# Kernel optimization log

Measured on AMD Instinct MI355X. Metric: run time of the kernel, lower is better.

Reference implementation:

```python
import jax, jax.numpy as jnp
import numpy as np

K = 20          # n_knn
BN_EPS = 1e-5   # torch BatchNorm2d default eps


def knn_idx(x, k):
    # x: (B, C, N). pairwise[b,i,j] = -||x_i||^2 + 2 x_i.x_j - ||x_j||^2 (neg sq dist)
    xx = jnp.sum(x * x, axis=1)                      # (B, N)
    inner = jnp.einsum('bci,bcj->bij', x, x)          # (B, N, N)
    pd = 2.0 * inner - xx[:, :, None] - xx[:, None, :]
    return jax.lax.top_k(pd, k)[1]                    # (B, N, k) nearest (incl. self)


def setup_inputs() -> dict:
    key = jax.random.key(0)
    k1, k2, k3, k4 = jax.random.split(key, 4)
    B, C, N, O = 8, 64, 2048, 128
    x = jax.random.normal(k1, (B, C, N), dtype=jnp.float32)
    W = jax.random.normal(k2, (O, 2 * C), dtype=jnp.float32) * 0.05  # conv1x1 weight, no bias
    gamma = 1.0 + 0.1 * jax.random.normal(k3, (O,), dtype=jnp.float32)
    beta = 0.1 * jax.random.normal(k4, (O,), dtype=jnp.float32)
    return {'x': x, 'W': W, 'gamma': gamma, 'beta': beta}


def reference(x, W, gamma, beta):
    # x: (B, C, N)
    idx = knn_idx(x, K)                               # (B, N, K) int32
    xt = jnp.swapaxes(x, 1, 2)                        # (B, N, C)
    nbr = jax.vmap(lambda xb, ib: xb[ib])(xt, idx)    # (B, N, K, C) gathered neighbors
    center = xt[:, :, None, :]                        # (B, N, 1, C)
    feat = jnp.concatenate(
        [nbr - center, jnp.broadcast_to(center, nbr.shape)], axis=-1
    )                                                 # (B, N, K, 2C)
    # 1x1 conv == per-edge GEMM
    h = jnp.einsum('bnkc,oc->bnko', feat, W)          # (B, N, K, O)
    # BatchNorm2d (training mode): batch stats over (B, N, K) per channel, biased var
    mean = jnp.mean(h, axis=(0, 1, 2))
    var = jnp.var(h, axis=(0, 1, 2))
    h = (h - mean) * jax.lax.rsqrt(var + BN_EPS) * gamma + beta
    h = jax.nn.gelu(h, approximate=False)             # torch nn.GELU exact erf form
    out = jnp.max(h, axis=2)                          # max over k neighbors -> (B, N, O)
    return jnp.swapaxes(out, 1, 2)                    # (B, O, N) matches torch layout
```

## Files before the change

### kernel.cpp

```cpp
#include <hip/hip_runtime.h>
#include <math.h>

#define BB 8
#define CC 64
#define NN 2048
#define KK 20
#define OO 128
#define CANDT 28
#define NPART 512
#define NPARTB 1024
#define M_TOT 327680.0f

typedef __attribute__((ext_vector_type(8))) __bf16 bf8v;
typedef __attribute__((ext_vector_type(16))) float f32x16;

__global__ __launch_bounds__(256, 4) void k_pqprep(const float* __restrict__ x,
                                                   const float* __restrict__ W,
                                                   float* __restrict__ P,
                                                   float* __restrict__ Q,
                                                   ushort* __restrict__ xT,
                                                   float* __restrict__ xTf,
                                                   double* __restrict__ xx,
                                                   float* __restrict__ xxf) {
  __shared__ float xs[32][68];
  __shared__ float Wl[OO][68];
  __shared__ float tile[32][OO + 1];
  const int t = threadIdx.x;
  const int jj = t & 31, og = t >> 5;
  const int pt0 = blockIdx.x * 32;
  const int b = pt0 >> 11;
  const int n0 = pt0 & (NN - 1);

#pragma unroll
  for (int r = 0; r < 2; ++r) {
    int seg = t + r * 256;
    int c = seg >> 3, n4 = (seg & 7) * 4;
    float4 v = *(const float4*)(x + ((size_t)(b * CC + c) << 11) + n0 + n4);
    xs[n4 + 0][c] = v.x; xs[n4 + 1][c] = v.y;
    xs[n4 + 2][c] = v.z; xs[n4 + 3][c] = v.w;
  }
#pragma unroll
  for (int r = 0; r < 8; ++r) {
    int seg = t + r * 256;
    int o = seg >> 4, c4 = (seg & 15) * 4;
    *(float4*)(&Wl[o][c4]) = *(const float4*)(W + (size_t)o * (2 * CC) + c4);
  }
  __syncthreads();

  float xcol[CC];
#pragma unroll
  for (int c = 0; c < CC; c += 4) {
    float4 v = *(const float4*)(&xs[jj][c]);
    xcol[c] = v.x; xcol[c + 1] = v.y; xcol[c + 2] = v.z; xcol[c + 3] = v.w;
  }

  if (t < 32) {
    int i = pt0 + t;
    ushort* rowp = xT + (size_t)i * CC;
    float* rowf = xTf + (size_t)i * CC;
    double s = 0.0;
#pragma unroll
    for (int c8 = 0; c8 < 8; ++c8) {
      unsigned tmp[8];
      float f[8];
#pragma unroll
      for (int e = 0; e < 8; ++e) {
        float v = xs[t][c8 * 8 + e];
// ... 96 lines not shown
    pk.w = tmp[6] | (tmp[7] << 16);
    *(uint4*)(rowp + c8 * 8) = pk;
    *(float4*)(rowf + c8 * 8)     = make_float4(f[0], f[1], f[2], f[3]);
    *(float4*)(rowf + c8 * 8 + 4) = make_float4(f[4], f[5], f[6], f[7]);
  }
  xx[i] = s;
  xxf[i] = (float)s;
}

__global__ __launch_bounds__(256) void k_pq(const float* __restrict__ x,
                                            const float* __restrict__ W,
                                            float* __restrict__ P,
                                            float* __restrict__ Q) {
  __shared__ float tile[64][OO + 1];
  const int t = threadIdx.x;
  const int jj = t & 63, og = t >> 6;
  const int pt0 = blockIdx.x * 64;
  const int b = pt0 >> 11;
  const int jn = (pt0 & (NN - 1)) + jj;

  float xcol[CC];
#pragma unroll
  for (int c = 0; c < CC; ++c) xcol[c] = x[((size_t)(b * CC + c) << 11) + jn];

  for (int oo = 0; oo < 32; ++oo) {
    int o = og * 32 + oo;
    const float* wr = W + (size_t)o * (2 * CC);
    float sp = 0.f;
#pragma unroll
    for (int c = 0; c < CC; ++c) sp = fmaf(wr[c], xcol[c], sp);
    tile[jj][o] = sp;
  }
  __syncthreads();
  for (int it = 0; it < 32; ++it) {
    int r = it * 2 + (t >> 7);
    P[((size_t)(pt0 + r)) * OO + (t & 127)] = tile[r][t & 127];
  }
  __syncthreads();
  for (int oo = 0; oo < 32; ++oo) {
    int o = og * 32 + oo;
    const float* wr = W + (size_t)o * (2 * CC);
    float sq = 0.f;
#pragma unroll
    for (int c = 0; c < CC; ++c) sq = fmaf(wr[CC + c] - wr[c], xcol[c], sq);
    tile[jj][o] = sq;
  }
  __syncthreads();
  for (int it = 0; it < 32; ++it) {
    int r = it * 2 + (t >> 7);
    Q[((size_t)(pt0 + r)) * OO + (t & 127)] = tile[r][t & 127];
  }
}

__global__ __launch_bounds__(1024, 4) void k_knn(
    const ushort* __restrict__ xT, const float* __restrict__ xxf,
    const float* __restrict__ xTf, const double* __restrict__ xx,
    int* __restrict__ idx, const float* __restrict__ P,
    const float* __restrict__ Q, float* __restrict__ partial,
    float* __restrict__ vmaxA, float* __restrict__ vminA) {
  extern __shared__ char smem[];
  ushort (*Sb)[NN] = (ushort(*)[NN])smem;
  int* Cj = (int*)(smem + 32 * NN * 2);
  double* Sd = (double*)(smem + 32 * NN * 2 + 4096);
  float* redF = (float*)Sd;
  int (*sIdxL)[KK] = (int(*)[KK])(smem + 32 * NN * 2 + 4096 + 8192);
  const int t = threadIdx.x;
  const int w = t >> 6, lane = t & 63;
  const int bidswz = ((blockIdx.x & 7) << 6) + (blockIdx.x >> 3);
  const int b = bidswz >> 6;
  const int i0 = (bidswz & 63) << 5;
  const int lr = lane & 31, lh = lane >> 5;
  const ushort* xTb = xT + (((size_t)b) << 11) * CC;

  f32x16 acc[4];
#pragma unroll
  for (int tt = 0; tt < 4; ++tt)
#pragma unroll
    for (int q = 0; q < 16; ++q) acc[tt][q] = 0.f;

  const ushort* Ap = xTb + (size_t)(i0 + lr) * CC + lh * 8;
  bf8v a0 = *(const bf8v*)(Ap);
  bf8v a1 = *(const bf8v*)(Ap + 16);
  bf8v a2 = *(const bf8v*)(Ap + 32);
  bf8v a3 = *(const bf8v*)(Ap + 48);
  const int j0w = w << 7;
#pragma unroll
  for (int tt = 0; tt < 4; ++tt) {
    const ushort* Bp = xTb + (size_t)(j0w + tt * 32 + lr) * CC + lh * 8;
    bf8v b0 = *(const bf8v*)(Bp);
    bf8v b1 = *(const bf8v*)(Bp + 16);
    bf8v b2 = *(const bf8v*)(Bp + 32);
    bf8v b3 = *(const bf8v*)(Bp + 48);
    acc[tt] = __builtin_amdgcn_mfma_f32_32x32x16_bf16(a0, b0, acc[tt], 0, 0, 0);
    acc[tt] = __builtin_amdgcn_mfma_f32_32x32x16_bf16(a1, b1, acc[tt], 0, 0, 0);
    acc[tt] = __builtin_amdgcn_mfma_f32_32x32x16_bf16(a2, b2, acc[tt], 0, 0, 0);
    acc[tt] = __builtin_amdgcn_mfma_f32_32x32x16_bf16(a3, b3, acc[tt], 0, 0, 0);
  }

  const float* xxfb = xxf + (b << 11);
#pragma unroll
  for (int tt = 0; tt < 4; ++tt) {
    int j = j0w + tt * 32 + lr;
    float xv = xxfb[j];
#pragma unroll
    for (int q = 0; q < 16; ++q) {
      int rr = (q & 3) + 8 * (q >> 2) + 4 * lh;
      float sv = fmaf(2.f, acc[tt][q], -xv);
      unsigned u = __float_as_uint(sv);
      u ^= (0x80000000u | (unsigned)((int)u >> 31));
      Sb[rr][j] = (ushort)(u >> 16);
    }
  }
  __syncthreads();

  const float* xTfb = xTf + (((size_t)b) << 11) * CC;
  const double* xxb = xx + (b << 11);
#pragma unroll 1
  for (int rw = 0; rw < 2; ++rw) {
    const int rr = w + 16 * rw;
    const int irow = i0 + rr;
    uint4 kq[4];
    unsigned t0 = 0, t1 = 0, t2 = 0, t3 = 0;
#pragma unroll
    for (int g = 0; g < 4; ++g) {
      uint4 raw = *(const uint4*)(&Sb[rr][lane * 8 + g * 512]);
      kq[g] = raw;
      const unsigned wds[4] = {raw.x, raw.y, raw.z, raw.w};
#pragma unroll
      for (int e = 0; e < 4; ++e) {
        unsigned k0 = wds[e] & 0xffffu, k1 = wds[e] >> 16;
        unsigned mx, mn;
        mx = k0 > t0 ? k0 : t0; mn = k0 > t0 ? t0 : k0; t0 = mx;
        mx = mn > t1 ? mn : t1; mn = mn > t1 ? t1 : mn; t1 = mx;
        mx = mn > t2 ? mn : t2; mn = mn > t2 ? t2 : mn; t2 = mx;
        t3 = mn > t3 ? mn : t3;
        mx = k1 > t0 ? k1 : t0; mn = k1 > t0 ? t0 : k1; t0 = mx;
        mx = mn > t1 ? mn : t1; mn = mn > t1 ? t1 : mn; t1 = mx;
        mx = mn > t2 ? mn : t2; mn = mn > t2 ? t2 : mn; t2 = mx;
        t3 = mn > t3 ? mn : t3;
      }
    }
    unsigned tau = 0;
    for (int bit = 15; bit >= 0; --bit) {
      unsigned cnd = tau | (1u << bit);
      int tot = __popcll(__ballot(t0 >= cnd)) + __popcll(__ballot(t1 >= cnd)) +
                __popcll(__ballot(t2 >= cnd)) + __popcll(__ballot(t3 >= cnd));
      if (tot >= CANDT) tau = cnd;
    }
    unsigned mask = 0;
#pragma unroll
    for (int g = 0; g < 4; ++g) {
      const unsigned wds[4] = {kq[g].x, kq[g].y, kq[g].z, kq[g].w};
#pragma unroll
      for (int e = 0; e < 4; ++e) {
        mask |= ((wds[e] & 0xffffu) >= tau ? 1u : 0u) << (g * 8 + e * 2);
        mask |= ((wds[e] >> 16) >= tau ? 1u : 0u) << (g * 8 + e * 2 + 1);
      }
    }
    int myc = __popc(mask);
    int pre = myc;
#pragma unroll
    for (int off = 1; off < 64; off <<= 1) {
      int o = __shfl_up(pre, off, 64);
      pre += (lane >= off) ? o : 0;
    }
    int tot = __shfl(pre, 63, 64);
    if (tot > 64) {
      tau = 0;
      for (int bit = 15; bit >= 0; --bit) {
        unsigned cnd = tau | (1u << bit);
        int cc = 0;
#pragma unroll
        for (int g = 0; g < 4; ++g) {
          const unsigned wds[4] = {kq[g].x, kq[g].y, kq[g].z, kq[g].w};
#pragma unroll
          for (int e = 0; e < 4; ++e) {
            cc += ((wds[e] & 0xffffu) >= cnd) ? 1 : 0;
            cc += ((wds[e] >> 16) >= cnd) ? 1 : 0;
          }
        }
#pragma unroll
        for (int off = 1; off < 64; off <<= 1) cc += __shfl_xor(cc, off, 64);
        if (cc >= CANDT) tau = cnd;
      }
      mask = 0;
#pragma unroll
      for (int g = 0; g < 4; ++g) {
        const unsigned wds[4] = {kq[g].x, kq[g].y, kq[g].z, kq[g].w};
#pragma unroll
        for (int e = 0; e < 4; ++e) {
          mask |= ((wds[e] & 0xffffu) >= tau ? 1u : 0u) << (g * 8 + e * 2);
          mask |= ((wds[e] >> 16) >= tau ? 1u : 0u) << (g * 8 + e * 2 + 1);
        }
      }
      myc = __popc(mask);
      pre = myc;
#pragma unroll
      for (int off = 1; off < 64; off <<= 1) {
        int o = __shfl_up(pre, off, 64);
        pre += (lane >= off) ? o : 0;
      }
      tot = __shfl(pre, 63, 64);
    }
    {
      int slot = pre - myc;
      unsigned m2 = mask;
      while (m2) {
        int bp = __builtin_ctz(m2); m2 &= m2 - 1;
        if (slot < 64) Cj[w * 64 + slot] = lane * 8 + ((bp >> 3) << 9) + (bp & 7);
        ++slot;
      }
    }
    int cnt = tot > 64 ? 64 : tot;
    int j = Cj[w * 64 + (lane < cnt ? lane : 0)];
    const float* xi = xTfb + (size_t)irow * CC;
    const float* xj = xTfb + (size_t)j * CC;
    double d0 = 0, d1 = 0, d2 = 0, d3 = 0;
#pragma unroll
    for (int c = 0; c < CC; c += 4) {
      float4 fi = *(const float4*)(xi + c);
      float4 fj = *(const float4*)(xj + c);
      d0 = fma((double)fi.x, (double)fj.x, d0);
      d1 = fma((double)fi.y, (double)fj.y, d1);
      d2 = fma((double)fi.z, (double)fj.z, d2);
      d3 = fma((double)fi.w, (double)fj.w, d3);
    }
    double sc = 2.0 * ((d0 + d1) + (d2 + d3)) - xxb[j];
    Sd[w * 64 + lane] = sc;
    int rank = 0;
#pragma unroll 4
    for (int mm = 0; mm < cnt; ++mm) {
      double sm = Sd[w * 64 + mm];
      int jm = Cj[w * 64 + mm];
      rank += (sm > sc || (sm == sc && jm < j)) ? 1 : 0;
    }
    if (lane < cnt && rank < KK) {
      idx[(size_t)((b << 11) + irow) * KK + rank] = j;
      sIdxL[rr][rank] = j;
    }
  }

  if (P != nullptr) {
    __syncthreads();
    const int grp = t >> 7;
    const int o = t & 127;
    float s = 0.f, s2 = 0.f;
#pragma unroll
    for (int pp = 0; pp < 4; ++pp) {
      const int pl = grp * 4 + pp;
      const int pt = (b << 11) + i0 + pl;
      float qv = Q[(size_t)pt * OO + o];
      float vmax = -3.0e38f, vmin = 3.0e38f;
#pragma unroll
      for (int k = 0; k < KK; ++k) {
        float v = P[((size_t)((b << 11) + sIdxL[pl][k])) * OO + o] + qv;
        s += v;
        s2 = fmaf(v, v, s2);
        vmax = fmaxf(vmax, v);
        vmin = fminf(vmin, v);
      }
      vmaxA[(size_t)pt * OO + o] = vmax;
      vminA[(size_t)pt * OO + o] = vmin;
    }
    redF[grp * 128 + o] = s;
    redF[1024 + grp * 128 + o] = s2;
    __syncthreads();
    if (t < 128) {
      float as = 0.f, as2 = 0.f;
#pragma unroll
      for (int g = 0; g < 8; ++g) {
        as  += redF[g * 128 + t];
        as2 += redF[1024 + g * 128 + t];
      }
      partial[(size_t)bidswz * 128 + t]               = as;
      partial[(size_t)NPART * 128 + (size_t)bidswz * 128 + t] = as2;
    }
  }
}

__global__ __launch_bounds__(256) void k_stats(const float* __restrict__ P,
                                               const float* __restrict__ Q,
                                               const int* __restrict__ idx,
                                               float* __restrict__ partial) {
  __shared__ int sIdx[16 * KK];
  __shared__ float red[512];
  const int t = threadIdx.x;
  const int o = t & 127, half = t >> 7;
  const int bid = (blockIdx.x & 7) * 128 + (blockIdx.x >> 3);
  const int pt0 = bid * 16;
  const int b = pt0 >> 11;
  if (t < 160)
    *(int2*)(sIdx + t * 2) = *(const int2*)(idx + (size_t)pt0 * KK + t * 2);
  __syncthreads();

  float s = 0.f, s2 = 0.f;
  for (int it = 0; it < 8; ++it) {
    int pl = it * 2 + half;
    int pt = pt0 + pl;
    float qv = Q[(size_t)pt * OO + o];
    const int* ip = sIdx + pl * KK;
#pragma unroll
    for (int k = 0; k < KK; ++k) {
// ... 53 lines not shown
  const float scale = ss[o], shift = ss[128 + o];
  const int pt0 = bid * 32;
  const int b = pt0 >> 11;
  const float inv_sqrt2 = 0.70710678118654752f;
  for (int it = 0; it < 16; ++it) {
    int pl = it * 2 + half;
    int pt = pt0 + pl;
    float vmax, vmin;
    if (use_minmax) {
      vmax = vmaxA[(size_t)pt * OO + o];
      vmin = vminA[(size_t)pt * OO + o];
    } else {
      float qv = Q[(size_t)pt * OO + o];
      const int* ip = idx + (size_t)pt * KK;
      vmax = -3.0e38f; vmin = 3.0e38f;
#pragma unroll
      for (int k = 0; k < KK; ++k) {
        float v = P[((size_t)((b << 11) + ip[k])) * OO + o] + qv;
        vmax = fmaxf(vmax, v);
        vmin = fminf(vmin, v);
      }
    }
    float ymax, ymin;
    if (scale >= 0.f) { ymax = fmaf(vmax, scale, shift); ymin = fmaf(vmin, scale, shift); }
    else              { ymax = fmaf(vmin, scale, shift); ymin = fmaf(vmax, scale, shift); }
    float g;
    if (ymax > 0.f) {
      g = 0.5f * ymax * (1.0f + erff(ymax * inv_sqrt2));
    } else {
      float g1 = 0.5f * ymax * (1.0f + erff(ymax * inv_sqrt2));
      float g2 = 0.5f * ymin * (1.0f + erff(ymin * inv_sqrt2));
      g = fmaxf(g1, g2);
    }
    tile[pl][o] = g;
  }
  __syncthreads();
  const int n0 = pt0 & (NN - 1);
  for (int rep = 0; rep < 16; ++rep) {
    int oo = rep * 8 + (t >> 5);
    int nn = t & 31;
    out[((size_t)(b * OO + oo) << 11) + n0 + nn] = tile[nn][oo];
  }
}

extern "C" void kernel_launch(void* const* d_in, const int* in_sizes, int n_in,
                              void* d_out, int out_size, void* d_ws, size_t ws_size,
                              hipStream_t stream) {
  const float* x     = (const float*)d_in[0];
  const float* W     = (const float*)d_in[1];
  const float* gamma = (const float*)d_in[2];
  const float* beta  = (const float*)d_in[3];
  float* out = (float*)d_out;

  const int knn_lds = 32 * NN * 2 + 4096 + 8192 + 32 * KK * 4;
  hipFuncSetAttribute((const void*)k_knn,
                      hipFuncAttributeMaxDynamicSharedMemorySize, knn_lds);

  const size_t needA = 131072 + 65536 + 1310720 + (size_t)2 * NPARTB * 128 * 4 +
                       1024 + 4ull * 8388608;

  if (ws_size >= needA) {
    double* xx   = (double*)d_ws;
    float*  xxf  = (float*)(xx + BB * NN);
    int*    idxp = (int*)(xxf + BB * NN);
    float*  part = (float*)(idxp + (size_t)BB * NN * KK);
    float*  ss   = part + 2 * NPARTB * 128;
    float*  P    = ss + 256;
    float*  Q    = P + (size_t)BB * NN * OO;
    ushort* xT   = (ushort*)(Q + (size_t)BB * NN * OO);
    float*  xTf  = (float*)(xT + (size_t)BB * NN * CC);
    float*  vmax = xTf + (size_t)BB * NN * CC;
    float*  vmin = vmax + (size_t)BB * NN * OO;
    const size_t needSafe = (size_t)((char*)(vmin + (size_t)BB * NN * OO) - (char*)d_ws);
    if (ws_size >= needSafe) {
      hipLaunchKernelGGL(k_pqprep, dim3(BB * NN / 32), dim3(256), 0, stream,
                         x, W, P, Q, xT, xTf, xx, xxf);
      hipLaunchKernelGGL(k_knn, dim3(BB * NN / 32), dim3(1024), knn_lds, stream,
                         xT, xxf, xTf, xx, idxp, P, Q, part, vmax, vmin);
      hipLaunchKernelGGL(k_fin, dim3(128), dim3(256), 0, stream, part, gamma, beta, ss, NPART);
      hipLaunchKernelGGL(k_out, dim3(BB * NN / 32), dim3(256), 0, stream,
                         P, Q, idxp, ss, vmax, vmin, 1, out);
      return;
    }
    ushort* xTa  = (ushort*)(Q + (size_t)BB * NN * OO);
    float*  xTfa = (float*)(xTa + (size_t)BB * NN * CC);
    hipLaunchKernelGGL(k_pqprep, dim3(BB * NN / 32), dim3(256), 0, stream,
                       x, W, P, Q, xTa, xTfa, xx, xxf);
    hipLaunchKernelGGL(k_knn, dim3(BB * NN / 32), dim3(1024), knn_lds, stream,
                       xTa, xxf, xTfa, xx, idxp,
                       (const float*)nullptr, (const float*)nullptr,
                       (float*)nullptr, (float*)nullptr, (float*)nullptr);
    hipLaunchKernelGGL(k_stats, dim3(NPARTB), dim3(256), 0, stream,
                       P, Q, idxp, part);
    hipLaunchKernelGGL(k_fin, dim3(128), dim3(256), 0, stream, part, gamma, beta, ss, NPARTB);
    hipLaunchKernelGGL(k_out, dim3(BB * NN / 32), dim3(256), 0, stream,
                       P, Q, idxp, ss, (const float*)nullptr, (const float*)nullptr, 0, out);
  } else {
    double* xx   = (double*)d_ws;
    int*    idxp = (int*)(xx + BB * NN);
    float*  P    = (float*)(idxp + (size_t)BB * NN * KK);
    float*  Q    = P + (size_t)BB * NN * OO;
    float*  part = Q + (size_t)BB * NN * OO;
    float*  ss   = part + 2 * NPARTB * 128;
    ushort* xT   = (ushort*)P;
    float*  xTf  = P + (size_t)BB * NN * (CC / 2);
    float*  xxf  = Q;

    hipLaunchKernelGGL(k_prep, dim3(BB * NN / 256), dim3(256), 0, stream,
                       x, xT, xTf, xx, xxf);
    hipLaunchKernelGGL(k_knn, dim3(BB * NN / 32), dim3(1024), knn_lds, stream,
                       xT, xxf, xTf, xx, idxp,
                       (const float*)nullptr, (const float*)nullptr,
                       (float*)nullptr, (float*)nullptr, (float*)nullptr);
    hipLaunchKernelGGL(k_pq, dim3(BB * NN / 64), dim3(256), 0, stream, x, W, P, Q);
    hipLaunchKernelGGL(k_stats, dim3(NPARTB), dim3(256), 0, stream,
                       P, Q, idxp, part);
    hipLaunchKernelGGL(k_fin, dim3(128), dim3(256), 0, stream, part, gamma, beta, ss, NPARTB);
    hipLaunchKernelGGL(k_out, dim3(BB * NN / 32), dim3(256), 0, stream,
                       P, Q, idxp, ss, (const float*)nullptr, (const float*)nullptr, 0, out);
  }
}
```

Before: 115.6 us.

## Interleave two KNN rows per wave and split MFMA score tiles into halves

Each wave now processes its two query rows together, interleaving their top-4 filtering, radix threshold search, prefix sums, fp64 rescoring and rank computation to expose more instruction-level parallelism and hide LDS and global latency. The MFMA score computation is split into two halves of two accumulators each, lowering peak register pressure. Candidate and score buffers in LDS are doubled to hold per-row data, which raises LDS use and may lower occupancy. The interleaved code also raises register demand in the selection phase.

```diff
diff --git a/kernel.cpp b/kernel.cpp
--- a/kernel.cpp
+++ b/kernel.cpp
@@ -215,6 +215,45 @@
   }
 }
 
+__device__ __forceinline__ void exact_radix_q(const uint4* kq, int lane,
+                                              unsigned& tau, unsigned& mask,
+                                              int& myc, int& pre, int& tot) {
+  tau = 0;
+  for (int bit = 15; bit >= 0; --bit) {
+    unsigned cnd = tau | (1u << bit);
+    int cc = 0;
+#pragma unroll
+    for (int g = 0; g < 4; ++g) {
+      const unsigned wds[4] = {kq[g].x, kq[g].y, kq[g].z, kq[g].w};
+#pragma unroll
+      for (int e = 0; e < 4; ++e) {
+        cc += ((wds[e] & 0xffffu) >= cnd) ? 1 : 0;
+        cc += ((wds[e] >> 16) >= cnd) ? 1 : 0;
+      }
+    }
+#pragma unroll
+    for (int off = 1; off < 64; off <<= 1) cc += __shfl_xor(cc, off, 64);
+    if (cc >= CANDT) tau = cnd;
+  }
+  mask = 0;
+#pragma unroll
+  for (int g = 0; g < 4; ++g) {
+    const unsigned wds[4] = {kq[g].x, kq[g].y, kq[g].z, kq[g].w};
+#pragma unroll
+    for (int e = 0; e < 4; ++e) {
+      mask |= ((wds[e] & 0xffffu) >= tau ? 1u : 0u) << (g * 8 + e * 2);
+      mask |= ((wds[e] >> 16) >= tau ? 1u : 0u) << (g * 8 + e * 2 + 1);
+    }
+  }
+  myc = __popc(mask); pre = myc;
+#pragma unroll
+  for (int off = 1; off < 64; off <<= 1) {
+    int o = __shfl_up(pre, off, 64);
+    pre += (lane >= off) ? o : 0;
+  }
+  tot = __shfl(pre, 63, 64);
+}
+
 __global__ __launch_bounds__(1024, 4) void k_knn(
     const ushort* __restrict__ xT, const float* __restrict__ xxf,
     const float* __restrict__ xTf, const double* __restrict__ xx,
@@ -223,10 +262,10 @@
     float* __restrict__ vmaxA, float* __restrict__ vminA) {
   extern __shared__ char smem[];
   ushort (*Sb)[NN] = (ushort(*)[NN])smem;
-  int* Cj = (int*)(smem + 32 * NN * 2);
-  double* Sd = (double*)(smem + 32 * NN * 2 + 4096);
-  float* redF = (float*)Sd;
-  int (*sIdxL)[KK] = (int(*)[KK])(smem + 32 * NN * 2 + 4096 + 8192);
+  int (*CjS)[64] = (int(*)[64])(smem + 32 * NN * 2);
+  double (*SdS)[64] = (double(*)[64])(smem + 32 * NN * 2 + 8192);
+  float* redF = (float*)SdS;
+  int (*sIdxL)[KK] = (int(*)[KK])(smem + 32 * NN * 2 + 8192 + 16384);
   const int t = threadIdx.x;
   const int w = t >> 6, lane = t & 63;
   const int bidswz = ((blockIdx.x & 7) << 6) + (blockIdx.x >> 3);
@@ -234,12 +273,7 @@
   const int i0 = (bidswz & 63) << 5;
   const int lr = lane & 31, lh = lane >> 5;
   const ushort* xTb = xT + (((size_t)b) << 11) * CC;
-
-  f32x16 acc[4];
-#pragma unroll
-  for (int tt = 0; tt < 4; ++tt)
-#pragma unroll
-    for (int q = 0; q < 16; ++q) acc[tt][q] = 0.f;
+  const float* xxfb = xxf + (b << 11);
 
   const ushort* Ap = xTb + (size_t)(i0 + lr) * CC + lh * 8;
   bf8v a0 = *(const bf8v*)(Ap);
@@ -247,160 +281,183 @@
   bf8v a2 = *(const bf8v*)(Ap + 32);
   bf8v a3 = *(const bf8v*)(Ap + 48);
   const int j0w = w << 7;
-#pragma unroll
-  for (int tt = 0; tt < 4; ++tt) {
-    const ushort* Bp = xTb + (size_t)(j0w + tt * 32 + lr) * CC + lh * 8;
-    bf8v b0 = *(const bf8v*)(Bp);
-    bf8v b1 = *(const bf8v*)(Bp + 16);
-    bf8v b2 = *(const bf8v*)(Bp + 32);
-    bf8v b3 = *(const bf8v*)(Bp + 48);
-    acc[tt] = __builtin_amdgcn_mfma_f32_32x32x16_bf16(a0, b0, acc[tt], 0, 0, 0);
-    acc[tt] = __builtin_amdgcn_mfma_f32_32x32x16_bf16(a1, b1, acc[tt], 0, 0, 0);
-    acc[tt] = __builtin_amdgcn_mfma_f32_32x32x16_bf16(a2, b2, acc[tt], 0, 0, 0);
-    acc[tt] = __builtin_amdgcn_mfma_f32_32x32x16_bf16(a3, b3, acc[tt], 0, 0, 0);
-  }
-
-  const float* xxfb = xxf + (b << 11);
-#pragma unroll
-  for (int tt = 0; tt < 4; ++tt) {
-    int j = j0w + tt * 32 + lr;
-    float xv = xxfb[j];
-#pragma unroll
-    for (int q = 0; q < 16; ++q) {
-      int rr = (q & 3) + 8 * (q >> 2) + 4 * lh;
-      float sv = fmaf(2.f, acc[tt][q], -xv);
-      unsigned u = __float_as_uint(sv);
-      u ^= (0x80000000u | (unsigned)((int)u >> 31));
-      Sb[rr][j] = (ushort)(u >> 16);
+#pragma unroll 1
+  for (int h = 0; h < 2; ++h) {
+    f32x16 acc2[2];
+#pragma unroll
+    for (int u = 0; u < 2; ++u)
+#pragma unroll
+      for (int q = 0; q < 16; ++q) acc2[u][q] = 0.f;
+#pragma unroll
+    for (int u = 0; u < 2; ++u) {
+      const int tt = h * 2 + u;
+      const ushort* Bp = xTb + (size_t)(j0w + tt * 32 + lr) * CC + lh * 8;
+      bf8v b0 = *(const bf8v*)(Bp);
+      bf8v b1 = *(const bf8v*)(Bp + 16);
+      bf8v b2 = *(const bf8v*)(Bp + 32);
+      bf8v b3 = *(const bf8v*)(Bp + 48);
+      acc2[u] = __builtin_amdgcn_mfma_f32_32x32x16_bf16(a0, b0, acc2[u], 0, 0, 0);
+      acc2[u] = __builtin_amdgcn_mfma_f32_32x32x16_bf16(a1, b1, acc2[u], 0, 0, 0);
+      acc2[u] = __builtin_amdgcn_mfma_f32_32x32x16_bf16(a2, b2, acc2[u], 0, 0, 0);
+      acc2[u] = __builtin_amdgcn_mfma_f32_32x32x16_bf16(a3, b3, acc2[u], 0, 0, 0);
+    }
+#pragma unroll
+    for (int u = 0; u < 2; ++u) {
+      const int tt = h * 2 + u;
+      int j = j0w + tt * 32 + lr;
+      float xv = xxfb[j];
+#pragma unroll
+      for (int q = 0; q < 16; ++q) {
+        int rr = (q & 3) + 8 * (q >> 2) + 4 * lh;
+        float sv = fmaf(2.f, acc2[u][q], -xv);
+        unsigned uu = __float_as_uint(sv);
+        uu ^= (0x80000000u | (unsigned)((int)uu >> 31));
+        Sb[rr][j] = (ushort)(uu >> 16);
+      }
     }
   }
   __syncthreads();
 
   const float* xTfb = xTf + (((size_t)b) << 11) * CC;
   const double* xxb = xx + (b << 11);
-#pragma unroll 1
-  for (int rw = 0; rw < 2; ++rw) {
-    const int rr = w + 16 * rw;
-    const int irow = i0 + rr;
-    uint4 kq[4];
-    unsigned t0 = 0, t1 = 0, t2 = 0, t3 = 0;
-#pragma unroll
-    for (int g = 0; g < 4; ++g) {
-      uint4 raw = *(const uint4*)(&Sb[rr][lane * 8 + g * 512]);
-      kq[g] = raw;
-      const unsigned wds[4] = {raw.x, raw.y, raw.z, raw.w};
-#pragma unroll
-      for (int e = 0; e < 4; ++e) {
-        unsigned k0 = wds[e] & 0xffffu, k1 = wds[e] >> 16;
-        unsigned mx, mn;
-        mx = k0 > t0 ? k0 : t0; mn = k0 > t0 ? t0 : k0; t0 = mx;
-        mx = mn > t1 ? mn : t1; mn = mn > t1 ? t1 : mn; t1 = mx;
-        mx = mn > t2 ? mn : t2; mn = mn > t2 ? t2 : mn; t2 = mx;
-        t3 = mn > t3 ? mn : t3;
-        mx = k1 > t0 ? k1 : t0; mn = k1 > t0 ? t0 : k1; t0 = mx;
-        mx = mn > t1 ? mn : t1; mn = mn > t1 ? t1 : mn; t1 = mx;
-        mx = mn > t2 ? mn : t2; mn = mn > t2 ? t2 : mn; t2 = mx;
-        t3 = mn > t3 ? mn : t3;
-      }
-    }
-    unsigned tau = 0;
-    for (int bit = 15; bit >= 0; --bit) {
-      unsigned cnd = tau | (1u << bit);
-      int tot = __popcll(__ballot(t0 >= cnd)) + __popcll(__ballot(t1 >= cnd)) +
-                __popcll(__ballot(t2 >= cnd)) + __popcll(__ballot(t3 >= cnd));
-      if (tot >= CANDT) tau = cnd;
-    }
-    unsigned mask = 0;
-#pragma unroll
-    for (int g = 0; g < 4; ++g) {
-      const unsigned wds[4] = {kq[g].x, kq[g].y, kq[g].z, kq[g].w};
-#pragma unroll
-      for (int e = 0; e < 4; ++e) {
-        mask |= ((wds[e] & 0xffffu) >= tau ? 1u : 0u) << (g * 8 + e * 2);
-        mask |= ((wds[e] >> 16) >= tau ? 1u : 0u) << (g * 8 + e * 2 + 1);
-      }
-    }
-    int myc = __popc(mask);
-    int pre = myc;
-#pragma unroll
-    for (int off = 1; off < 64; off <<= 1) {
-      int o = __shfl_up(pre, off, 64);
-      pre += (lane >= off) ? o : 0;
-    }
-    int tot = __shfl(pre, 63, 64);
-    if (tot > 64) {
-      tau = 0;
-      for (int bit = 15; bit >= 0; --bit) {
-        unsigned cnd = tau | (1u << bit);
-        int cc = 0;
-#pragma unroll
-        for (int g = 0; g < 4; ++g) {
-          const unsigned wds[4] = {kq[g].x, kq[g].y, kq[g].z, kq[g].w};
-#pragma unroll
-          for (int e = 0; e < 4; ++e) {
-            cc += ((wds[e] & 0xffffu) >= cnd) ? 1 : 0;
-            cc += ((wds[e] >> 16) >= cnd) ? 1 : 0;
-          }
-        }
-#pragma unroll
-        for (int off = 1; off < 64; off <<= 1) cc += __shfl_xor(cc, off, 64);
-        if (cc >= CANDT) tau = cnd;
-      }
-      mask = 0;
-#pragma unroll
-      for (int g = 0; g < 4; ++g) {
-        const unsigned wds[4] = {kq[g].x, kq[g].y, kq[g].z, kq[g].w};
-#pragma unroll
-        for (int e = 0; e < 4; ++e) {
-          mask |= ((wds[e] & 0xffffu) >= tau ? 1u : 0u) << (g * 8 + e * 2);
-          mask |= ((wds[e] >> 16) >= tau ? 1u : 0u) << (g * 8 + e * 2 + 1);
-        }
-      }
-      myc = __popc(mask);
-      pre = myc;
-#pragma unroll
-      for (int off = 1; off < 64; off <<= 1) {
-        int o = __shfl_up(pre, off, 64);
-        pre += (lane >= off) ? o : 0;
-      }
-      tot = __shfl(pre, 63, 64);
-    }
-    {
-      int slot = pre - myc;
-      unsigned m2 = mask;
-      while (m2) {
-        int bp = __builtin_ctz(m2); m2 &= m2 - 1;
-        if (slot < 64) Cj[w * 64 + slot] = lane * 8 + ((bp >> 3) << 9) + (bp & 7);
-        ++slot;
-      }
-    }
-    int cnt = tot > 64 ? 64 : tot;
-    int j = Cj[w * 64 + (lane < cnt ? lane : 0)];
-    const float* xi = xTfb + (size_t)irow * CC;
-    const float* xj = xTfb + (size_t)j * CC;
-    double d0 = 0, d1 = 0, d2 = 0, d3 = 0;
-#pragma unroll
-    for (int c = 0; c < CC; c += 4) {
-      float4 fi = *(const float4*)(xi + c);
-      float4 fj = *(const float4*)(xj + c);
-      d0 = fma((double)fi.x, (double)fj.x, d0);
-      d1 = fma((double)fi.y, (double)fj.y, d1);
-      d2 = fma((double)fi.z, (double)fj.z, d2);
-      d3 = fma((double)fi.w, (double)fj.w, d3);
-    }
-    double sc = 2.0 * ((d0 + d1) + (d2 + d3)) - xxb[j];
-    Sd[w * 64 + lane] = sc;
-    int rank = 0;
-#pragma unroll 4
-    for (int mm = 0; mm < cnt; ++mm) {
-      double sm = Sd[w * 64 + mm];
-      int jm = Cj[w * 64 + mm];
-      rank += (sm > sc || (sm == sc && jm < j)) ? 1 : 0;
-    }
-    if (lane < cnt && rank < KK) {
-      idx[(size_t)((b << 11) + irow) * KK + rank] = j;
-      sIdxL[rr][rank] = j;
-    }
+  const int rrA = w, rrB = w + 16;
+  const int irowA = i0 + rrA, irowB = i0 + rrB;
+
+  uint4 kqA[4], kqB[4];
+  unsigned tA0 = 0, tA1 = 0, tA2 = 0, tA3 = 0;
+  unsigned tB0 = 0, tB1 = 0, tB2 = 0, tB3 = 0;
+#pragma unroll
+  for (int g = 0; g < 4; ++g) {
+    uint4 rawA = *(const uint4*)(&Sb[rrA][lane * 8 + g * 512]);
+    uint4 rawB = *(const uint4*)(&Sb[rrB][lane * 8 + g * 512]);
+    kqA[g] = rawA; kqB[g] = rawB;
+    const unsigned wA[4] = {rawA.x, rawA.y, rawA.z, rawA.w};
+    const unsigned wB[4] = {rawB.x, rawB.y, rawB.z, rawB.w};
+#pragma unroll
+    for (int e = 0; e < 4; ++e) {
+      unsigned kA0 = wA[e] & 0xffffu, kA1 = wA[e] >> 16;
+      unsigned kB0 = wB[e] & 0xffffu, kB1 = wB[e] >> 16;
+      unsigned mx, mn;
+      mx = kA0 > tA0 ? kA0 : tA0; mn = kA0 > tA0 ? tA0 : kA0; tA0 = mx;
+      mx = mn > tA1 ? mn : tA1; mn = mn > tA1 ? tA1 : mn; tA1 = mx;
+      mx = mn > tA2 ? mn : tA2; mn = mn > tA2 ? tA2 : mn; tA2 = mx;
+      tA3 = mn > tA3 ? mn : tA3;
+      mx = kB0 > tB0 ? kB0 : tB0; mn = kB0 > tB0 ? tB0 : kB0; tB0 = mx;
+      mx = mn > tB1 ? mn : tB1; mn = mn > tB1 ? tB1 : mn; tB1 = mx;
+      mx = mn > tB2 ? mn : tB2; mn = mn > tB2 ? tB2 : mn; tB2 = mx;
+      tB3 = mn > tB3 ? mn : tB3;
+      mx = kA1 > tA0 ? kA1 : tA0; mn = kA1 > tA0 ? tA0 : kA1; tA0 = mx;
+      mx = mn > tA1 ? mn : tA1; mn = mn > tA1 ? tA1 : mn; tA1 = mx;
+      mx = mn > tA2 ? mn : tA2; mn = mn > tA2 ? tA2 : mn; tA2 = mx;
+      tA3 = mn > tA3 ? mn : tA3;
+      mx = kB1 > tB0 ? kB1 : tB0; mn = kB1 > tB0 ? tB0 : kB1; tB0 = mx;
+      mx = mn > tB1 ? mn : tB1; mn = mn > tB1 ? tB1 : mn; tB1 = mx;
+      mx = mn > tB2 ? mn : tB2; mn = mn > tB2 ? tB2 : mn; tB2 = mx;
+      tB3 = mn > tB3 ? mn : tB3;
+    }
+  }
+  unsigned tauA = 0, tauB = 0;
+  for (int bit = 15; bit >= 0; --bit) {
+    unsigned cA = tauA | (1u << bit), cB = tauB | (1u << bit);
+    int totA_ = __popcll(__ballot(tA0 >= cA)) + __popcll(__ballot(tA1 >= cA)) +
+                __popcll(__ballot(tA2 >= cA)) + __popcll(__ballot(tA3 >= cA));
+    int totB_ = __popcll(__ballot(tB0 >= cB)) + __popcll(__ballot(tB1 >= cB)) +
+                __popcll(__ballot(tB2 >= cB)) + __popcll(__ballot(tB3 >= cB));
+    if (totA_ >= CANDT) tauA = cA;
+    if (totB_ >= CANDT) tauB = cB;
+  }
+  unsigned maskA = 0, maskB = 0;
+#pragma unroll
+  for (int g = 0; g < 4; ++g) {
+    const unsigned wA[4] = {kqA[g].x, kqA[g].y, kqA[g].z, kqA[g].w};
+    const unsigned wB[4] = {kqB[g].x, kqB[g].y, kqB[g].z, kqB[g].w};
+#pragma unroll
+    for (int e = 0; e < 4; ++e) {
+      maskA |= ((wA[e] & 0xffffu) >= tauA ? 1u : 0u) << (g * 8 + e * 2);
+      maskA |= ((wA[e] >> 16) >= tauA ? 1u : 0u) << (g * 8 + e * 2 + 1);
+      maskB |= ((wB[e] & 0xffffu) >= tauB ? 1u : 0u) << (g * 8 + e * 2);
+      maskB |= ((wB[e] >> 16) >= tauB ? 1u : 0u) << (g * 8 + e * 2 + 1);
+    }
+  }
+  int mycA = __popc(maskA), mycB = __popc(maskB);
+  int preA = mycA, preB = mycB;
+#pragma unroll
+  for (int off = 1; off < 64; off <<= 1) {
+    int oA = __shfl_up(preA, off, 64);
+    int oB = __shfl_up(preB, off, 64);
+    preA += (lane >= off) ? oA : 0;
+    preB += (lane >= off) ? oB : 0;
+  }
+  int totA = __shfl(preA, 63, 64);
+  int totB = __shfl(preB, 63, 64);
+  if (totA > 64) exact_radix_q(kqA, lane, tauA, maskA, mycA, preA, totA);
+  if (totB > 64) exact_radix_q(kqB, lane, tauB, maskB, mycB, preB, totB);
+  {
+    int slot = preA - mycA;
+    unsigned m2 = maskA;
+    while (m2) {
+      int bp = __builtin_ctz(m2); m2 &= m2 - 1;
+      if (slot < 64) CjS[rrA][slot] = lane * 8 + ((bp >> 3) << 9) + (bp & 7);
+      ++slot;
+    }
+  }
+  {
+    int slot = preB - mycB;
+    unsigned m2 = maskB;
+    while (m2) {
+      int bp = __builtin_ctz(m2); m2 &= m2 - 1;
+      if (slot < 64) CjS[rrB][slot] = lane * 8 + ((bp >> 3) << 9) + (bp & 7);
+      ++slot;
+    }
+  }
+  const int cntA = totA > 64 ? 64 : totA;
+  const int cntB = totB > 64 ? 64 : totB;
+
+  int jA = CjS[rrA][lane < cntA ? lane : 0];
+  int jB = CjS[rrB][lane < cntB ? lane : 0];
+  const float* xiA = xTfb + (size_t)irowA * CC;
+  const float* xiB = xTfb + (size_t)irowB * CC;
+  const float* xjA = xTfb + (size_t)jA * CC;
+  const float* xjB = xTfb + (size_t)jB * CC;
+  double dA0 = 0, dA1 = 0, dA2 = 0, dA3 = 0;
+  double dB0 = 0, dB1 = 0, dB2 = 0, dB3 = 0;
+#pragma unroll
+  for (int c = 0; c < CC; c += 4) {
+    float4 fiA = *(const float4*)(xiA + c);
+    float4 fjA = *(const float4*)(xjA + c);
+    float4 fiB = *(const float4*)(xiB + c);
+    float4 fjB = *(const float4*)(xjB + c);
+    dA0 = fma((double)fiA.x, (double)fjA.x, dA0);
+    dB0 = fma((double)fiB.x, (double)fjB.x, dB0);
+    dA1 = fma((double)fiA.y, (double)fjA.y, dA1);
+    dB1 = fma((double)fiB.y, (double)fjB.y, dB1);
+    dA2 = fma((double)fiA.z, (double)fjA.z, dA2);
+    dB2 = fma((double)fiB.z, (double)fjB.z, dB2);
+    dA3 = fma((double)fiA.w, (double)fjA.w, dA3);
+    dB3 = fma((double)fiB.w, (double)fjB.w, dB3);
+  }
+  double scA = 2.0 * ((dA0 + dA1) + (dA2 + dA3)) - xxb[jA];
+  double scB = 2.0 * ((dB0 + dB1) + (dB2 + dB3)) - xxb[jB];
+
+  SdS[rrA][lane] = scA;
+  SdS[rrB][lane] = scB;
+  int rankA = 0, rankB = 0;
+  const int cmax = cntA > cntB ? cntA : cntB;
+  for (int mm = 0; mm < cmax; ++mm) {
+    int mA = mm < cntA ? mm : 0;
+    int mB = mm < cntB ? mm : 0;
+    double smA = SdS[rrA][mA]; int jmA = CjS[rrA][mA];
+    double smB = SdS[rrB][mB]; int jmB = CjS[rrB][mB];
+    if (mm < cntA) rankA += (smA > scA || (smA == scA && jmA < jA)) ? 1 : 0;
+    if (mm < cntB) rankB += (smB > scB || (smB == scB && jmB < jB)) ? 1 : 0;
+  }
+  if (lane < cntA && rankA < KK) {
+    idx[(size_t)((b << 11) + irowA) * KK + rankA] = jA;
+    sIdxL[rrA][rankA] = jA;
+  }
+  if (lane < cntB && rankB < KK) {
+    idx[(size_t)((b << 11) + irowB) * KK + rankB] = jB;
+    sIdxL[rrB][rankB] = jB;
   }
 
   if (P != nullptr) {
@@ -570,7 +627,7 @@
   const float* beta  = (const float*)d_in[3];
   float* out = (float*)d_out;
 
-  const int knn_lds = 32 * NN * 2 + 4096 + 8192 + 32 * KK * 4;
+  const int knn_lds = 32 * NN * 2 + 8192 + 16384 + 32 * KK * 4;
   hipFuncSetAttribute((const void*)k_knn,
                       hipFuncAttributeMaxDynamicSharedMemorySize, knn_lds);
 
```

Measured after the change: 110.5 us (median of 2 runs). 1.05x faster.

## Shrink kNN block to 16 query rows using 16x16 MFMA tiles

Applied to the files above, without the earlier changes.

The kNN kernel now handles 16 query rows per block instead of 32. It switches from 32x32x16 to 16x16x32 bf16 MFMA, computed in two halves so each wave keeps fewer accumulators live. The LDS score buffer halves, the grid doubles, launch bounds allow more resident blocks, and each wave now selects one row instead of looping over two. The fused stats path is adjusted to two points per group with NPART raised to match. The aim is higher occupancy and lower register and LDS pressure, at the cost of reloading the B operand more often across blocks and launching more blocks.

```diff
diff --git a/kernel.cpp b/kernel.cpp
--- a/kernel.cpp
+++ b/kernel.cpp
@@ -7,12 +7,12 @@
 #define KK 20
 #define OO 128
 #define CANDT 28
-#define NPART 512
+#define NPART 1024
 #define NPARTB 1024
 #define M_TOT 327680.0f
 
 typedef __attribute__((ext_vector_type(8))) __bf16 bf8v;
-typedef __attribute__((ext_vector_type(16))) float f32x16;
+typedef __attribute__((ext_vector_type(4))) float f32x4;
 
 __global__ __launch_bounds__(256, 4) void k_pqprep(const float* __restrict__ x,
                                                    const float* __restrict__ W,
@@ -215,7 +215,46 @@
   }
 }
 
-__global__ __launch_bounds__(1024, 4) void k_knn(
+__device__ __forceinline__ void exact_radix_q(const uint4* kq, int lane,
+                                              unsigned& tau, unsigned& mask,
+                                              int& myc, int& pre, int& tot) {
+  tau = 0;
+  for (int bit = 15; bit >= 0; --bit) {
+    unsigned cnd = tau | (1u << bit);
+    int cc = 0;
+#pragma unroll
+    for (int g = 0; g < 4; ++g) {
+      const unsigned wds[4] = {kq[g].x, kq[g].y, kq[g].z, kq[g].w};
+#pragma unroll
+      for (int e = 0; e < 4; ++e) {
+        cc += ((wds[e] & 0xffffu) >= cnd) ? 1 : 0;
+        cc += ((wds[e] >> 16) >= cnd) ? 1 : 0;
+      }
+    }
+#pragma unroll
+    for (int off = 1; off < 64; off <<= 1) cc += __shfl_xor(cc, off, 64);
+    if (cc >= CANDT) tau = cnd;
+  }
+  mask = 0;
+#pragma unroll
+  for (int g = 0; g < 4; ++g) {
+    const unsigned wds[4] = {kq[g].x, kq[g].y, kq[g].z, kq[g].w};
+#pragma unroll
+    for (int e = 0; e < 4; ++e) {
+      mask |= ((wds[e] & 0xffffu) >= tau ? 1u : 0u) << (g * 8 + e * 2);
+      mask |= ((wds[e] >> 16) >= tau ? 1u : 0u) << (g * 8 + e * 2 + 1);
+    }
+  }
+  myc = __popc(mask); pre = myc;
+#pragma unroll
+  for (int off = 1; off < 64; off <<= 1) {
+    int o = __shfl_up(pre, off, 64);
+    pre += (lane >= off) ? o : 0;
+  }
+  tot = __shfl(pre, 63, 64);
+}
+
+__global__ __launch_bounds__(1024, 8) void k_knn(
     const ushort* __restrict__ xT, const float* __restrict__ xxf,
     const float* __restrict__ xTf, const double* __restrict__ xx,
     int* __restrict__ idx, const float* __restrict__ P,
@@ -223,184 +262,143 @@
     float* __restrict__ vmaxA, float* __restrict__ vminA) {
   extern __shared__ char smem[];
   ushort (*Sb)[NN] = (ushort(*)[NN])smem;
-  int* Cj = (int*)(smem + 32 * NN * 2);
-  double* Sd = (double*)(smem + 32 * NN * 2 + 4096);
-  float* redF = (float*)Sd;
-  int (*sIdxL)[KK] = (int(*)[KK])(smem + 32 * NN * 2 + 4096 + 8192);
+  int (*CjS)[64] = (int(*)[64])(smem + 16 * NN * 2);
+  double (*SdS)[64] = (double(*)[64])(smem + 16 * NN * 2 + 4096);
+  float* redF = (float*)SdS;
+  int (*sIdxL)[KK] = (int(*)[KK])(smem + 16 * NN * 2 + 4096 + 8192);
   const int t = threadIdx.x;
   const int w = t >> 6, lane = t & 63;
-  const int bidswz = ((blockIdx.x & 7) << 6) + (blockIdx.x >> 3);
-  const int b = bidswz >> 6;
-  const int i0 = (bidswz & 63) << 5;
-  const int lr = lane & 31, lh = lane >> 5;
+  const int bidswz = ((blockIdx.x & 7) << 7) + (blockIdx.x >> 3);
+  const int b = bidswz >> 7;
+  const int i0 = (bidswz & 127) << 4;
+  const int lr16 = lane & 15, kg = lane >> 4;
   const ushort* xTb = xT + (((size_t)b) << 11) * CC;
-
-  f32x16 acc[4];
-#pragma unroll
-  for (int tt = 0; tt < 4; ++tt)
-#pragma unroll
-    for (int q = 0; q < 16; ++q) acc[tt][q] = 0.f;
-
-  const ushort* Ap = xTb + (size_t)(i0 + lr) * CC + lh * 8;
-  bf8v a0 = *(const bf8v*)(Ap);
-  bf8v a1 = *(const bf8v*)(Ap + 16);
-  bf8v a2 = *(const bf8v*)(Ap + 32);
-  bf8v a3 = *(const bf8v*)(Ap + 48);
+  const float* xxfb = xxf + (b << 11);
+
+  const ushort* Arow = xTb + (size_t)(i0 + lr16) * CC + kg * 8;
+  bf8v aF0 = *(const bf8v*)(Arow);
+  bf8v aF1 = *(const bf8v*)(Arow + 32);
   const int j0w = w << 7;
-#pragma unroll
-  for (int tt = 0; tt < 4; ++tt) {
-    const ushort* Bp = xTb + (size_t)(j0w + tt * 32 + lr) * CC + lh * 8;
-    bf8v b0 = *(const bf8v*)(Bp);
-    bf8v b1 = *(const bf8v*)(Bp + 16);
-    bf8v b2 = *(const bf8v*)(Bp + 32);
-    bf8v b3 = *(const bf8v*)(Bp + 48);
-    acc[tt] = __builtin_amdgcn_mfma_f32_32x32x16_bf16(a0, b0, acc[tt], 0, 0, 0);
-    acc[tt] = __builtin_amdgcn_mfma_f32_32x32x16_bf16(a1, b1, acc[tt], 0, 0, 0);
-    acc[tt] = __builtin_amdgcn_mfma_f32_32x32x16_bf16(a2, b2, acc[tt], 0, 0, 0);
-    acc[tt] = __builtin_amdgcn_mfma_f32_32x32x16_bf16(a3, b3, acc[tt], 0, 0, 0);
-  }
-
-  const float* xxfb = xxf + (b << 11);
-#pragma unroll
-  for (int tt = 0; tt < 4; ++tt) {
-    int j = j0w + tt * 32 + lr;
-    float xv = xxfb[j];
-#pragma unroll
-    for (int q = 0; q < 16; ++q) {
-      int rr = (q & 3) + 8 * (q >> 2) + 4 * lh;
-      float sv = fmaf(2.f, acc[tt][q], -xv);
-      unsigned u = __float_as_uint(sv);
-      u ^= (0x80000000u | (unsigned)((int)u >> 31));
-      Sb[rr][j] = (ushort)(u >> 16);
+#pragma unroll 1
+  for (int h = 0; h < 2; ++h) {
+    f32x4 acc4[4];
+#pragma unroll
+    for (int u = 0; u < 4; ++u)
+#pragma unroll
+      for (int q = 0; q < 4; ++q) acc4[u][q] = 0.f;
+#pragma unroll
+    for (int u = 0; u < 4; ++u) {
+      const int ct = h * 4 + u;
+      const ushort* Brow = xTb + (size_t)(j0w + ct * 16 + lr16) * CC + kg * 8;
+      bf8v bF0 = *(const bf8v*)(Brow);
+      bf8v bF1 = *(const bf8v*)(Brow + 32);
+      acc4[u] = __builtin_amdgcn_mfma_f32_16x16x32_bf16(aF0, bF0, acc4[u], 0, 0, 0);
+      acc4[u] = __builtin_amdgcn_mfma_f32_16x16x32_bf16(aF1, bF1, acc4[u], 0, 0, 0);
+    }
+#pragma unroll
+    for (int u = 0; u < 4; ++u) {
+      const int ct = h * 4 + u;
+      int j = j0w + ct * 16 + lr16;
+      float xv = xxfb[j];
+#pragma unroll
+      for (int q = 0; q < 4; ++q) {
+        int rr = kg * 4 + q;
+        float sv = fmaf(2.f, acc4[u][q], -xv);
+        unsigned uu = __float_as_uint(sv);
+        uu ^= (0x80000000u | (unsigned)((int)uu >> 31));
+        Sb[rr][j] = (ushort)(uu >> 16);
+      }
     }
   }
   __syncthreads();
 
   const float* xTfb = xTf + (((size_t)b) << 11) * CC;
   const double* xxb = xx + (b << 11);
-#pragma unroll 1
-  for (int rw = 0; rw < 2; ++rw) {
-    const int rr = w + 16 * rw;
-    const int irow = i0 + rr;
-    uint4 kq[4];
-    unsigned t0 = 0, t1 = 0, t2 = 0, t3 = 0;
-#pragma unroll
-    for (int g = 0; g < 4; ++g) {
-      uint4 raw = *(const uint4*)(&Sb[rr][lane * 8 + g * 512]);
-      kq[g] = raw;
-      const unsigned wds[4] = {raw.x, raw.y, raw.z, raw.w};
-#pragma unroll
-      for (int e = 0; e < 4; ++e) {
-        unsigned k0 = wds[e] & 0xffffu, k1 = wds[e] >> 16;
-        unsigned mx, mn;
-        mx = k0 > t0 ? k0 : t0; mn = k0 > t0 ? t0 : k0; t0 = mx;
-        mx = mn > t1 ? mn : t1; mn = mn > t1 ? t1 : mn; t1 = mx;
-        mx = mn > t2 ? mn : t2; mn = mn > t2 ? t2 : mn; t2 = mx;
-        t3 = mn > t3 ? mn : t3;
-        mx = k1 > t0 ? k1 : t0; mn = k1 > t0 ? t0 : k1; t0 = mx;
-        mx = mn > t1 ? mn : t1; mn = mn > t1 ? t1 : mn; t1 = mx;
-        mx = mn > t2 ? mn : t2; mn = mn > t2 ? t2 : mn; t2 = mx;
-        t3 = mn > t3 ? mn : t3;
-      }
-    }
-    unsigned tau = 0;
-    for (int bit = 15; bit >= 0; --bit) {
-      unsigned cnd = tau | (1u << bit);
-      int tot = __popcll(__ballot(t0 >= cnd)) + __popcll(__ballot(t1 >= cnd)) +
-                __popcll(__ballot(t2 >= cnd)) + __popcll(__ballot(t3 >= cnd));
-      if (tot >= CANDT) tau = cnd;
-    }
-    unsigned mask = 0;
-#pragma unroll
-    for (int g = 0; g < 4; ++g) {
-      const unsigned wds[4] = {kq[g].x, kq[g].y, kq[g].z, kq[g].w};
-#pragma unroll
-      for (int e = 0; e < 4; ++e) {
-        mask |= ((wds[e] & 0xffffu) >= tau ? 1u : 0u) << (g * 8 + e * 2);
-        mask |= ((wds[e] >> 16) >= tau ? 1u : 0u) << (g * 8 + e * 2 + 1);
-      }
-    }
-    int myc = __popc(mask);
-    int pre = myc;
-#pragma unroll
-    for (int off = 1; off < 64; off <<= 1) {
-      int o = __shfl_up(pre, off, 64);
-      pre += (lane >= off) ? o : 0;
-    }
-    int tot = __shfl(pre, 63, 64);
-    if (tot > 64) {
-      tau = 0;
-      for (int bit = 15; bit >= 0; --bit) {
-        unsigned cnd = tau | (1u << bit);
-        int cc = 0;
-#pragma unroll
-        for (int g = 0; g < 4; ++g) {
-          const unsigned wds[4] = {kq[g].x, kq[g].y, kq[g].z, kq[g].w};
-#pragma unroll
-          for (int e = 0; e < 4; ++e) {
-            cc += ((wds[e] & 0xffffu) >= cnd) ? 1 : 0;
-            cc += ((wds[e] >> 16) >= cnd) ? 1 : 0;
-          }
-        }
-#pragma unroll
-        for (int off = 1; off < 64; off <<= 1) cc += __shfl_xor(cc, off, 64);
-        if (cc >= CANDT) tau = cnd;
-      }
-      mask = 0;
-#pragma unroll
-      for (int g = 0; g < 4; ++g) {
-        const unsigned wds[4] = {kq[g].x, kq[g].y, kq[g].z, kq[g].w};
-#pragma unroll
-        for (int e = 0; e < 4; ++e) {
-          mask |= ((wds[e] & 0xffffu) >= tau ? 1u : 0u) << (g * 8 + e * 2);
-          mask |= ((wds[e] >> 16) >= tau ? 1u : 0u) << (g * 8 + e * 2 + 1);
-        }
-      }
-      myc = __popc(mask);
-      pre = myc;
-#pragma unroll
-      for (int off = 1; off < 64; off <<= 1) {
-        int o = __shfl_up(pre, off, 64);
-        pre += (lane >= off) ? o : 0;
-      }
-      tot = __shfl(pre, 63, 64);
-    }
-    {
-      int slot = pre - myc;
-      unsigned m2 = mask;
-      while (m2) {
-        int bp = __builtin_ctz(m2); m2 &= m2 - 1;
-        if (slot < 64) Cj[w * 64 + slot] = lane * 8 + ((bp >> 3) << 9) + (bp & 7);
-        ++slot;
-      }
-    }
-    int cnt = tot > 64 ? 64 : tot;
-    int j = Cj[w * 64 + (lane < cnt ? lane : 0)];
-    const float* xi = xTfb + (size_t)irow * CC;
-    const float* xj = xTfb + (size_t)j * CC;
-    double d0 = 0, d1 = 0, d2 = 0, d3 = 0;
-#pragma unroll
-    for (int c = 0; c < CC; c += 4) {
-      float4 fi = *(const float4*)(xi + c);
-      float4 fj = *(const float4*)(xj + c);
-      d0 = fma((double)fi.x, (double)fj.x, d0);
-      d1 = fma((double)fi.y, (double)fj.y, d1);
-      d2 = fma((double)fi.z, (double)fj.z, d2);
-      d3 = fma((double)fi.w, (double)fj.w, d3);
-    }
-    double sc = 2.0 * ((d0 + d1) + (d2 + d3)) - xxb[j];
-    Sd[w * 64 + lane] = sc;
-    int rank = 0;
+  const int rr = w;
+  const int irow = i0 + rr;
+
+  uint4 kq[4];
+  unsigned t0 = 0, t1 = 0, t2 = 0, t3 = 0;
+#pragma unroll
+  for (int g = 0; g < 4; ++g) {
+    uint4 raw = *(const uint4*)(&Sb[rr][lane * 8 + g * 512]);
+    kq[g] = raw;
+    const unsigned wds[4] = {raw.x, raw.y, raw.z, raw.w};
+#pragma unroll
+    for (int e = 0; e < 4; ++e) {
+      unsigned k0 = wds[e] & 0xffffu, k1 = wds[e] >> 16;
+      unsigned mx, mn;
+      mx = k0 > t0 ? k0 : t0; mn = k0 > t0 ? t0 : k0; t0 = mx;
+      mx = mn > t1 ? mn : t1; mn = mn > t1 ? t1 : mn; t1 = mx;
+      mx = mn > t2 ? mn : t2; mn = mn > t2 ? t2 : mn; t2 = mx;
+      t3 = mn > t3 ? mn : t3;
+      mx = k1 > t0 ? k1 : t0; mn = k1 > t0 ? t0 : k1; t0 = mx;
+      mx = mn > t1 ? mn : t1; mn = mn > t1 ? t1 : mn; t1 = mx;
+      mx = mn > t2 ? mn : t2; mn = mn > t2 ? t2 : mn; t2 = mx;
+      t3 = mn > t3 ? mn : t3;
+    }
+  }
+  unsigned tau = 0;
+  for (int bit = 15; bit >= 0; --bit) {
+    unsigned cnd = tau | (1u << bit);
+    int tot_ = __popcll(__ballot(t0 >= cnd)) + __popcll(__ballot(t1 >= cnd)) +
+               __popcll(__ballot(t2 >= cnd)) + __popcll(__ballot(t3 >= cnd));
+    if (tot_ >= CANDT) tau = cnd;
+  }
+  unsigned mask = 0;
+#pragma unroll
+  for (int g = 0; g < 4; ++g) {
+    const unsigned wds[4] = {kq[g].x, kq[g].y, kq[g].z, kq[g].w};
+#pragma unroll
+    for (int e = 0; e < 4; ++e) {
+      mask |= ((wds[e] & 0xffffu) >= tau ? 1u : 0u) << (g * 8 + e * 2);
+      mask |= ((wds[e] >> 16) >= tau ? 1u : 0u) << (g * 8 + e * 2 + 1);
+    }
+  }
+  int myc = __popc(mask);
+  int pre = myc;
+#pragma unroll
+  for (int off = 1; off < 64; off <<= 1) {
+    int o = __shfl_up(pre, off, 64);
+    pre += (lane >= off) ? o : 0;
+  }
+  int tot = __shfl(pre, 63, 64);
+  if (tot > 64) exact_radix_q(kq, lane, tau, mask, myc, pre, tot);
+  {
+    int slot = pre - myc;
+    unsigned m2 = mask;
+    while (m2) {
+      int bp = __builtin_ctz(m2); m2 &= m2 - 1;
+      if (slot < 64) CjS[rr][slot] = lane * 8 + ((bp >> 3) << 9) + (bp & 7);
+      ++slot;
+    }
+  }
+  const int cnt = tot > 64 ? 64 : tot;
+  int j = CjS[rr][lane < cnt ? lane : 0];
+  const float* xi = xTfb + (size_t)irow * CC;
+  const float* xj = xTfb + (size_t)j * CC;
+  double d0 = 0, d1 = 0, d2 = 0, d3 = 0;
+#pragma unroll
+  for (int c = 0; c < CC; c += 4) {
+    float4 fi = *(const float4*)(xi + c);
+    float4 fj = *(const float4*)(xj + c);
+    d0 = fma((double)fi.x, (double)fj.x, d0);
+    d1 = fma((double)fi.y, (double)fj.y, d1);
+    d2 = fma((double)fi.z, (double)fj.z, d2);
+    d3 = fma((double)fi.w, (double)fj.w, d3);
+  }
+  double sc = 2.0 * ((d0 + d1) + (d2 + d3)) - xxb[j];
+  SdS[rr][lane] = sc;
+  int rank = 0;
 #pragma unroll 4
-    for (int mm = 0; mm < cnt; ++mm) {
-      double sm = Sd[w * 64 + mm];
-      int jm = Cj[w * 64 + mm];
-      rank += (sm > sc || (sm == sc && jm < j)) ? 1 : 0;
-    }
-    if (lane < cnt && rank < KK) {
-      idx[(size_t)((b << 11) + irow) * KK + rank] = j;
-      sIdxL[rr][rank] = j;
-    }
+  for (int mm = 0; mm < cnt; ++mm) {
+    double sm = SdS[rr][mm];
+    int jm = CjS[rr][mm];
+    rank += (sm > sc || (sm == sc && jm < j)) ? 1 : 0;
+  }
+  if (lane < cnt && rank < KK) {
+    idx[(size_t)((b << 11) + irow) * KK + rank] = j;
+    sIdxL[rr][rank] = j;
   }
 
   if (P != nullptr) {
@@ -409,8 +407,8 @@
     const int o = t & 127;
     float s = 0.f, s2 = 0.f;
 #pragma unroll
-    for (int pp = 0; pp < 4; ++pp) {
-      const int pl = grp * 4 + pp;
+    for (int pp = 0; pp < 2; ++pp) {
+      const int pl = grp * 2 + pp;
       const int pt = (b << 11) + i0 + pl;
       float qv = Q[(size_t)pt * OO + o];
       float vmax = -3.0e38f, vmin = 3.0e38f;
@@ -570,7 +568,7 @@
   const float* beta  = (const float*)d_in[3];
   float* out = (float*)d_out;
 
-  const int knn_lds = 32 * NN * 2 + 4096 + 8192 + 32 * KK * 4;
+  const int knn_lds = 16 * NN * 2 + 4096 + 8192 + 16 * KK * 4;
   hipFuncSetAttribute((const void*)k_knn,
                       hipFuncAttributeMaxDynamicSharedMemorySize, knn_lds);
 
@@ -593,7 +591,7 @@
     if (ws_size >= needSafe) {
       hipLaunchKernelGGL(k_pqprep, dim3(BB * NN / 32), dim3(256), 0, stream,
                          x, W, P, Q, xT, xTf, xx, xxf);
-      hipLaunchKernelGGL(k_knn, dim3(BB * NN / 32), dim3(1024), knn_lds, stream,
+      hipLaunchKernelGGL(k_knn, dim3(BB * NN / 16), dim3(1024), knn_lds, stream,
                          xT, xxf, xTf, xx, idxp, P, Q, part, vmax, vmin);
       hipLaunchKernelGGL(k_fin, dim3(128), dim3(256), 0, stream, part, gamma, beta, ss, NPART);
       hipLaunchKernelGGL(k_out, dim3(BB * NN / 32), dim3(256), 0, stream,
@@ -604,7 +602,7 @@
     float*  xTfa = (float*)(xTa + (size_t)BB * NN * CC);
     hipLaunchKernelGGL(k_pqprep, dim3(BB * NN / 32), dim3(256), 0, stream,
                        x, W, P, Q, xTa, xTfa, xx, xxf);
-    hipLaunchKernelGGL(k_knn, dim3(BB * NN / 32), dim3(1024), knn_lds, stream,
+    hipLaunchKernelGGL(k_knn, dim3(BB * NN / 16), dim3(1024), knn_lds, stream,
                        xTa, xxf, xTfa, xx, idxp,
                        (const float*)nullptr, (const float*)nullptr,
                        (float*)nullptr, (float*)nullptr, (float*)nullptr);
@@ -626,7 +624,7 @@
 
     hipLaunchKernelGGL(k_prep, dim3(BB * NN / 256), dim3(256), 0, stream,
                        x, xT, xTf, xx, xxf);
-    hipLaunchKernelGGL(k_knn, dim3(BB * NN / 32), dim3(1024), knn_lds, stream,
+    hipLaunchKernelGGL(k_knn, dim3(BB * NN / 16), dim3(1024), knn_lds, stream,
                        xT, xxf, xTf, xx, idxp,
                        (const float*)nullptr, (const float*)nullptr,
                        (float*)nullptr, (float*)nullptr, (float*)nullptr);
```

New measurement: 130.2 us. 1.13x slower.
